# Optimization experiments

Measured on AMD Instinct MI355X. Metric: run time of the kernel, lower is better.

## Reference

```python
import jax, jax.numpy as jnp
import numpy as np

N = 50000   # nodes
E = 800000  # edges (before self-loops)
B = 256     # graphs in batch
F = 128     # input feature dim
H = 4       # heads per layer
C = 64      # out_channels per head
NEG_SLOPE = 0.2


def setup_inputs() -> dict:
    key = jax.random.key(0)
    ks = jax.random.split(key, 16)
    s = 0.05
    inp = {
        "x": jax.random.normal(ks[0], (N, F), dtype=jnp.float32),
        "edge_index": jax.random.randint(ks[1], (2, E), 0, N, dtype=jnp.int32),
        "batch": jnp.sort(jax.random.randint(ks[2], (N,), 0, B, dtype=jnp.int32)),
        # layer 1: F -> H*C
        "W1": jax.random.normal(ks[3], (F, H * C), dtype=jnp.float32) * s,
        "as1": jax.random.normal(ks[4], (H, C), dtype=jnp.float32) * s,
        "ad1": jax.random.normal(ks[5], (H, C), dtype=jnp.float32) * s,
        "b1": jnp.zeros((H * C,), dtype=jnp.float32),
        # layer 2: H*C -> H*C
        "W2": jax.random.normal(ks[6], (H * C, H * C), dtype=jnp.float32) * s,
        "as2": jax.random.normal(ks[7], (H, C), dtype=jnp.float32) * s,
        "ad2": jax.random.normal(ks[8], (H, C), dtype=jnp.float32) * s,
        "b2": jnp.zeros((H * C,), dtype=jnp.float32),
        # layer 3: H*C -> H*C
        "W3": jax.random.normal(ks[9], (H * C, H * C), dtype=jnp.float32) * s,
        "as3": jax.random.normal(ks[10], (H, C), dtype=jnp.float32) * s,
        "ad3": jax.random.normal(ks[11], (H, C), dtype=jnp.float32) * s,
        "b3": jnp.zeros((H * C,), dtype=jnp.float32),
    }
    return inp


def _gat_layer(x, src, dst, W, a_src, a_dst, bias):
    """PyG GATConv (concat=True, self-loops already included in src/dst)."""
    n = x.shape[0]
    xh = (x @ W).reshape(n, H, C)                      # [N,H,C]
    alpha_s = jnp.sum(xh * a_src, axis=-1)             # [N,H]
    alpha_d = jnp.sum(xh * a_dst, axis=-1)             # [N,H]
    logits = alpha_s[src] + alpha_d[dst]               # [E',H]
    logits = jnp.where(logits > 0, logits, NEG_SLOPE * logits)  # LeakyReLU
    # segment-wise softmax over destination neighborhoods
    m = jax.lax.stop_gradient(jax.ops.segment_max(logits, dst, num_segments=n))
    e = jnp.exp(logits - m[dst])
    z = jax.ops.segment_sum(e, dst, num_segments=n)
    alpha = e / (z[dst] + 1e-16)                       # [E',H]
    msg = xh[src] * alpha[:, :, None]                  # [E',H,C]
    out = jax.ops.segment_sum(msg, dst, num_segments=n)  # [N,H,C]
    return out.reshape(n, H * C) + bias


def reference(x, edge_index, batch, W1, as1, ad1, b1, W2, as2, ad2, b2, W3, as3, ad3, b3):
    n = x.shape[0]
    loops = jnp.arange(n, dtype=edge_index.dtype)
    src = jnp.concatenate([edge_index[0], loops])
    dst = jnp.concatenate([edge_index[1], loops])
    # dropout is identity at inference; activation = ReLU between layers
    h = jax.nn.relu(_gat_layer(x, src, dst, W1, as1, ad1, b1))
    h = jax.nn.relu(_gat_layer(h, src, dst, W2, as2, ad2, b2))
    h = _gat_layer(h, src, dst, W3, as3, ad3, b3)
    pooled = jax.ops.segment_max(h, batch, num_segments=B)  # global max pool -> [B, H*C]
    return jnp.squeeze(pooled)
```

## Files before the change

### kernel.cpp

```cpp
#include <hip/hip_runtime.h>
#include <hip/hip_fp16.h>
#include <math.h>

#define NN 50000
#define NE 800000
#define NT 850000
#define NB 256
#define FIN 128
#define HC 256
#define NH 4
#define CD 64
#define NEG 0.2f
#define SCAN_B 196

typedef _Float16 half8 __attribute__((ext_vector_type(8)));
typedef _Float16 half4v __attribute__((ext_vector_type(4)));
typedef float f32x4 __attribute__((ext_vector_type(4)));

__device__ __forceinline__ void gld16(const void* g, void* l) {
    __builtin_amdgcn_global_load_lds(
        (const __attribute__((address_space(1))) void*)g,
        (__attribute__((address_space(3))) void*)l, 16, 0, 0);
}


__global__ void zero_int_kernel(int* __restrict__ p, int n) {
    int i = blockIdx.x * blockDim.x + threadIdx.x;
    if (i < n) p[i] = 0;
}

__global__ void hist_kernel(const int* __restrict__ ei, int* __restrict__ cnt) {
    int e = blockIdx.x * blockDim.x + threadIdx.x;
    if (e < NE) {
        atomicAdd(&cnt[ei[NE + e]], 1);
    } else if (e < NT) {
        atomicAdd(&cnt[e - NE], 1);
    }
}

__global__ __launch_bounds__(256) void part_kernel(const int* __restrict__ cnt,
                                                   int* __restrict__ part) {
    __shared__ int red[4];
    int i = blockIdx.x * 256 + threadIdx.x;
    int v = (i < NN) ? cnt[i] : 0;
#pragma unroll
    for (int off = 32; off > 0; off >>= 1) v += __shfl_down(v, off);
    if ((threadIdx.x & 63) == 0) red[threadIdx.x >> 6] = v;
    __syncthreads();
    if (threadIdx.x == 0) part[blockIdx.x] = red[0] + red[1] + red[2] + red[3];
}

__global__ __launch_bounds__(256) void offs_kernel(const int* __restrict__ part,
                                                   int* __restrict__ boff) {
    __shared__ int sh[256];
    int t = threadIdx.x;
    sh[t] = (t < SCAN_B) ? part[t] : 0;
    __syncthreads();
    for (int off = 1; off < 256; off <<= 1) {
        int add = (t >= off) ? sh[t - off] : 0;
        __syncthreads();
        sh[t] += add;
        __syncthreads();
    }
    boff[t] = (t == 0) ? 0 : sh[t - 1];
}

__global__ __launch_bounds__(256) void write_scan_kernel(const int* __restrict__ cnt,
        const int* __restrict__ boff, int* __restrict__ rowptr, int* __restrict__ cursor) {
    __shared__ int sh[256];
    int t = threadIdx.x;
    int i = blockIdx.x * 256 + t;
    int v = (i < NN) ? cnt[i] : 0;
    sh[t] = v;
    __syncthreads();
    for (int off = 1; off < 256; off <<= 1) {
        int add = (t >= off) ? sh[t - off] : 0;
        __syncthreads();
        sh[t] += add;
        __syncthreads();
    }
    int run = boff[blockIdx.x] + sh[t] - v;
    if (i < NN) { rowptr[i] = run; cursor[i] = run; }
    if (i == NN - 1) rowptr[NN] = run + v;
}

__global__ void scatter_kernel(const int* __restrict__ ei, int* __restrict__ cursor,
                               int* __restrict__ colsrc, int* __restrict__ coldst) {
    int e = blockIdx.x * blockDim.x + threadIdx.x;
    int s, d;
    if (e < NE)      { s = ei[e]; d = ei[NE + e]; }
    else if (e < NT) { s = e - NE; d = s; }
    else return;
    int pos = atomicAdd(&cursor[d], 1);
    colsrc[pos] = s;
    coldst[pos] = d;
}

__global__ void batch_bounds_kernel(const int* __restrict__ batch, int* __restrict__ bstart) {
    int i = blockIdx.x * blockDim.x + threadIdx.x;
    if (i >= NN) return;
    int b = batch[i];
    if (i == 0) {
        for (int bb = 0; bb <= b; ++bb) bstart[bb] = 0;
    } else {
        int pb = batch[i - 1];
        if (pb != b) for (int bb = pb + 1; bb <= b; ++bb) bstart[bb] = i;
    }
    if (i == NN - 1) {
        for (int bb = b + 1; bb <= NB; ++bb) bstart[bb] = NN;
    }
}


__global__ __launch_bounds__(256) void split_x_kernel(const float* __restrict__ X,
        _Float16* __restrict__ Xh, _Float16* __restrict__ Xl) {
    int i = blockIdx.x * 256 + threadIdx.x;
    if (i >= NN * FIN / 4) return;
    float4 v = reinterpret_cast<const float4*>(X)[i];
    half4v h, l;
    h[0] = (_Float16)v.x; h[1] = (_Float16)v.y; h[2] = (_Float16)v.z; h[3] = (_Float16)v.w;
    l[0] = (_Float16)(v.x - (float)h[0]);
    l[1] = (_Float16)(v.y - (float)h[1]);
    l[2] = (_Float16)(v.z - (float)h[2]);
    l[3] = (_Float16)(v.w - (float)h[3]);
    reinterpret_cast<half4v*>(Xh)[i] = h;
    reinterpret_cast<half4v*>(Xl)[i] = l;
}


template<int K>
__global__ __launch_bounds__(256) void wprep_kernel(const float* __restrict__ W,
                                                    _Float16* __restrict__ WtS) {
    __shared__ float sm[8][257];
    const int t = threadIdx.x;
    const int b = blockIdx.x;
    const int kb = b * 8;
    const bool lo3 = (kb >= 2 * K);
    const int kphys = lo3 ? kb - 2 * K : (kb >= K ? kb - K : kb);
#pragma unroll
    for (int i = 0; i < 8; ++i) {
        int idx = i * 256 + t;
        sm[idx >> 8][idx & 255] = W[(size_t)(kphys + (idx >> 8)) * HC + (idx & 255)];
    }
    __syncthreads();
    half8 o;
#pragma unroll
    for (int r = 0; r < 8; ++r) {
        float w = sm[r][t];
        _Float16 h = (_Float16)w;
        o[r] = lo3 ? (_Float16)(w - (float)h) : h;
    }
    *reinterpret_cast<half8*>(&WtS[((size_t)b * 256 + t) * 8]) = o;
}


template<int K>
__global__ __launch_bounds__(256) void mfma_gemm_kernel(
        const _Float16* __restrict__ Xh, const _Float16* __restrict__ Xl,
        const _Float16* __restrict__ WtS, __half* __restrict__ XHo) {
    constexpr int C3 = 3 * K;
    constexpr int NSTEP = C3 / 64;
    __shared__ __align__(16) _Float16 As[2][64 * 64];
    __shared__ __align__(16) _Float16 Bs[2][64 * 256];
    const int t = threadIdx.x;
    const int lane = t & 63;
    const int wid = t >> 6;
    const int wm = wid & 1, wn = wid >> 1;
    const int r0 = blockIdx.x * 64;
    const int l15 = lane & 15;
    const int kcl = lane >> 4;
    const int srowA = t >> 3;
    const int skcA  = t & 7;

    f32x4 acc[2][8];
#pragma unroll
    for (int i = 0; i < 2; ++i)
#pragma unroll
        for (int j = 0; j < 8; ++j) acc[i][j] = (f32x4)0.f;

    auto loadA = [&](int s, float4& a0, float4& a1) {
        const int ks = s * 64;
        const _Float16* src = (ks < K) ? Xh : (ks < 2 * K) ? Xl : Xh;
        const int cbase = (ks < K) ? ks : (ks < 2 * K) ? ks - K : ks - 2 * K;
        a0 = *reinterpret_cast<const float4*>(src + (size_t)(r0 + srowA) * K + cbase + skcA * 8);
        a1 = *reinterpret_cast<const float4*>(src + (size_t)(r0 + 32 + srowA) * K + cbase + skcA * 8);
    };
    auto issueB = [&](int s, int buf) {
        const _Float16* bsrc = WtS + (size_t)s * (64 * 256);
#pragma unroll
        for (int r = 0; r < 8; ++r)
            gld16(bsrc + (r * 256 + t) * 8, &Bs[buf][(r * 256 + t) * 8]);
    };

    float4 va0, va1, vb0, vb1;
    loadA(0, va0, va1);
    issueB(0, 0);
    *reinterpret_cast<float4*>(&As[0][(skcA * 64 + ((srowA)      ^ skcA)) * 8]) = va0;
    *reinterpret_cast<float4*>(&As[0][(skcA * 64 + ((srowA + 32) ^ skcA)) * 8]) = va1;
    __syncthreads();

    for (int s = 0; s < NSTEP; ++s) {
        const int cur = s & 1, nxt = cur ^ 1;
        const bool more = (s + 1) < NSTEP;
        if (more) {
            loadA(s + 1, vb0, vb1);
            issueB(s + 1, nxt);
        }
#pragma unroll
        for (int kk = 0; kk < 2; ++kk) {
            const int kc = kk * 4 + kcl;
            half8 a0 = *reinterpret_cast<const half8*>(
                &As[cur][(kc * 64 + ((wm * 32      + l15) ^ kc)) * 8]);
            half8 a1 = *reinterpret_cast<const half8*>(
                &As[cur][(kc * 64 + ((wm * 32 + 16 + l15) ^ kc)) * 8]);
            const _Float16* bp = &Bs[cur][(kc * 256 + wn * 128 + l15) * 8];
#pragma unroll
            for (int nf = 0; nf < 8; ++nf) {
                half8 b = *reinterpret_cast<const half8*>(bp + nf * 16 * 8);
                acc[0][nf] = __builtin_amdgcn_mfma_f32_16x16x32_f16(a0, b, acc[0][nf], 0, 0, 0);
                acc[1][nf] = __builtin_amdgcn_mfma_f32_16x16x32_f16(a1, b, acc[1][nf], 0, 0, 0);
            }
        }
        if (more) {
            *reinterpret_cast<float4*>(&As[nxt][(skcA * 64 + ((srowA)      ^ skcA)) * 8]) = vb0;
            *reinterpret_cast<float4*>(&As[nxt][(skcA * 64 + ((srowA + 32) ^ skcA)) * 8]) = vb1;
        }
        asm volatile("s_waitcnt vmcnt(0) lgkmcnt(0)" ::: "memory");
        __builtin_amdgcn_s_barrier();
        __builtin_amdgcn_sched_barrier(0);
    }
    const int rb = r0 + wm * 32 + (lane >> 4) * 4;
    const int cb = wn * 128 + l15;
#pragma unroll
    for (int mf = 0; mf < 2; ++mf)
#pragma unroll
        for (int nf = 0; nf < 8; ++nf)
#pragma unroll
            for (int r = 0; r < 4; ++r) {
                int row = rb + mf * 16 + r;
                if (row < NN)
                    XHo[(size_t)row * HC + cb + nf * 16] = __float2half(acc[mf][nf][r]);
            }
}


__global__ __launch_bounds__(256) void alpha_kernel(const __half* __restrict__ XH,
        const float* __restrict__ as, const float* __restrict__ ad,
        float* __restrict__ aS, float* __restrict__ aD) {
    int r = blockIdx.x * 8 + (threadIdx.x >> 5);
    int g = threadIdx.x & 31;
    int h = g >> 3, sub = g & 7;
    half8 xv = *reinterpret_cast<const half8*>(XH + (size_t)r * HC + h * CD + sub * 8);
    const float* ap = as + h * CD + sub * 8;
    const float* dp = ad + h * CD + sub * 8;
    float s = 0.f, d = 0.f;
#pragma unroll
    for (int e = 0; e < 8; ++e) {
        float v = (float)xv[e];
        s += v * ap[e];
        d += v * dp[e];
    }
#pragma unroll
    for (int off = 1; off < 8; off <<= 1) {
        s += __shfl_xor(s, off);
        d += __shfl_xor(d, off);
    }
    if (sub == 0) { aS[r * NH + h] = s; aD[r * NH + h] = d; }
}


#define LEAKY(v) ((v) > 0.f ? (v) : NEG * (v))

__global__ __launch_bounds__(256) void ew_kernel(const int* __restrict__ colsrc,
        const int* __restrict__ coldst,
        const float* __restrict__ aS, const float* __restrict__ aD,
        float4* __restrict__ wE) {
    int p = blockIdx.x * blockDim.x + threadIdx.x;
    if (p >= NT) return;
    int s = colsrc[p], d = coldst[p];
    float4 sv = *reinterpret_cast<const float4*>(aS + s * 4);
    float4 dv = *reinterpret_cast<const float4*>(aD + d * 4);
    float4 w;
    w.x = __expf(LEAKY(sv.x + dv.x));
    w.y = __expf(LEAKY(sv.y + dv.y));
    w.z = __expf(LEAKY(sv.z + dv.z));
    w.w = __expf(LEAKY(sv.w + dv.w));
    wE[p] = w;
}


template<int RELU, int SPLIT>
__global__ __launch_bounds__(256) void aggregate_kernel(
        const int* __restrict__ rowptr, const int* __restrict__ colsrc,
        const float4* __restrict__ wE, const __half* __restrict__ XH,
        const float* __restrict__ bias, float* __restrict__ OUT,
        __half* __restrict__ OUTh, __half* __restrict__ OUTl) {
    int n = blockIdx.x * 4 + (threadIdx.x >> 6);
    int lane = threadIdx.x & 63;
    bool lo = lane < 32;
    const __half2* xbase = reinterpret_cast<const __half2*>(XH);
    float zl = 0.f, zh = 0.f;
    float al0 = 0.f, al1 = 0.f, ah0 = 0.f, ah1 = 0.f;
    int jb = rowptr[n], je = rowptr[n + 1];
    int j = jb;
    for (; j + 8 <= je; j += 8) {
        int sidx[8];
#pragma unroll
        for (int u = 0; u < 8; ++u) sidx[u] = colsrc[j + u];
        float4 w[8];
#pragma unroll
        for (int u = 0; u < 8; ++u) w[u] = wE[j + u];
        __half2 p[8], q[8];
#pragma unroll
        for (int u = 0; u < 8; ++u) {
            const __half2* xp = xbase + (size_t)sidx[u] * (HC / 2) + lane;
            p[u] = xp[0];
            q[u] = xp[64];
        }
#pragma unroll
        for (int u = 0; u < 8; ++u) {
            float wl = lo ? w[u].x : w[u].y, wh = lo ? w[u].z : w[u].w;
            float2 f = __half22float2(p[u]);
            al0 += wl * f.x; al1 += wl * f.y;
            f = __half22float2(q[u]);
            ah0 += wh * f.x; ah1 += wh * f.y;
            zl += wl; zh += wh;
        }
    }
    for (; j + 4 <= je; j += 4) {
        int sidx[4];
#pragma unroll
        for (int u = 0; u < 4; ++u) sidx[u] = colsrc[j + u];
        float4 w[4];
#pragma unroll
        for (int u = 0; u < 4; ++u) w[u] = wE[j + u];
        __half2 p[4], q[4];
#pragma unroll
        for (int u = 0; u < 4; ++u) {
            const __half2* xp = xbase + (size_t)sidx[u] * (HC / 2) + lane;
            p[u] = xp[0];
            q[u] = xp[64];
        }
#pragma unroll
        for (int u = 0; u < 4; ++u) {
            float wl = lo ? w[u].x : w[u].y, wh = lo ? w[u].z : w[u].w;
            float2 f = __half22float2(p[u]);
            al0 += wl * f.x; al1 += wl * f.y;
            f = __half22float2(q[u]);
            ah0 += wh * f.x; ah1 += wh * f.y;
            zl += wl; zh += wh;
        }
    }
    for (; j < je; ++j) {
        int s0 = colsrc[j];
        float4 w0 = wE[j];
        const __half2* xp = xbase + (size_t)s0 * (HC / 2) + lane;
        __half2 p0 = xp[0], q0 = xp[64];
        float w0l = lo ? w0.x : w0.y, w0h = lo ? w0.z : w0.w;
        float2 f = __half22float2(p0);
        al0 += w0l * f.x; al1 += w0l * f.y;
        f = __half22float2(q0);
        ah0 += w0h * f.x; ah1 += w0h * f.y;
        zl += w0l; zh += w0h;
    }
    float izl = 1.f / (zl + 1e-16f), izh = 1.f / (zh + 1e-16f);
    float2 bl = reinterpret_cast<const float2*>(bias)[lane];
    float2 bh = reinterpret_cast<const float2*>(bias + 128)[lane];
    float o0 = al0 * izl + bl.x;
    float o1 = al1 * izl + bl.y;
    float o2 = ah0 * izh + bh.x;
    float o3 = ah1 * izh + bh.y;
    if (RELU) {
        o0 = fmaxf(o0, 0.f); o1 = fmaxf(o1, 0.f);
        o2 = fmaxf(o2, 0.f); o3 = fmaxf(o3, 0.f);
    }
    if (SPLIT) {
        __half h0 = __float2half(o0), h1 = __float2half(o1);
        __half h2 = __float2half(o2), h3 = __float2half(o3);
        __half2* ph = reinterpret_cast<__half2*>(OUTh + (size_t)n * HC) + lane;
        ph[0]  = __half2(h0, h1);
        ph[64] = __half2(h2, h3);
        __half2* pl = reinterpret_cast<__half2*>(OUTl + (size_t)n * HC) + lane;
        pl[0]  = __half2(__float2half(o0 - __half2float(h0)), __float2half(o1 - __half2float(h1)));
        pl[64] = __half2(__float2half(o2 - __half2float(h2)), __float2half(o3 - __half2float(h3)));
    } else {
        float2* op = reinterpret_cast<float2*>(OUT + (size_t)n * HC) + lane;
        op[0]  = make_float2(o0, o1);
        op[64] = make_float2(o2, o3);
    }
}


__global__ __launch_bounds__(256) void pool_kernel(const float* __restrict__ Hf,
        const int* __restrict__ bstart, float* __restrict__ out) {
    int b = blockIdx.x;
    int c = threadIdx.x;
    int i0 = bstart[b], i1 = bstart[b + 1];
    float m = -INFINITY;
    for (int i = i0; i < i1; ++i) m = fmaxf(m, Hf[(size_t)i * HC + c]);
    out[b * HC + c] = m;
}


extern "C" void kernel_launch(void* const* d_in, const int* in_sizes, int n_in,
                              void* d_out, int out_size, void* d_ws, size_t ws_size,
                              hipStream_t stream) {
    const float* x     = (const float*)d_in[0];
    const int*   ei    = (const int*)d_in[1];
    const int*   batch = (const int*)d_in[2];
    const float* W1  = (const float*)d_in[3];
    const float* as1 = (const float*)d_in[4];
    const float* ad1 = (const float*)d_in[5];
    const float* b1  = (const float*)d_in[6];
    const float* W2  = (const float*)d_in[7];
    const float* as2 = (const float*)d_in[8];
    const float* ad2 = (const float*)d_in[9];
    const float* b2  = (const float*)d_in[10];
    const float* W3  = (const float*)d_in[11];
    const float* as3 = (const float*)d_in[12];
    const float* ad3 = (const float*)d_in[13];
    const float* b3  = (const float*)d_in[14];
    float* out = (float*)d_out;

    __half* Hh  = (__half*)d_ws;
    __half* Hl  = Hh + (size_t)NN * HC;
    __half* XHh = Hl + (size_t)NN * HC;
    _Float16* Xh1 = (_Float16*)Hh;
    _Float16* Xl1 = Xh1 + (size_t)NN * FIN;
    float* bufB = (float*)Hh;
    _Float16* WtS = (_Float16*)(XHh + (size_t)NN * HC);
    float4* wE  = (float4*)(WtS + 768 * 256);
    float*  aS  = (float*)(wE + NT);
    float*  aD  = aS + NN * NH;
    int* cnt    = (int*)(aD + NN * NH);
    int* rowptr = cnt + NN;
    int* cursor = rowptr + (NN + 1);
    int* colsrc = cursor + NN;
    int* coldst = colsrc + NT;
    int* bstart = coldst + NT;
    int* part   = bstart + (NB + 1);
    int* boff   = part + SCAN_B;

    zero_int_kernel<<<(NN + 255) / 256, 256, 0, stream>>>(cnt, NN);
    hist_kernel<<<(NT + 255) / 256, 256, 0, stream>>>(ei, cnt);
    part_kernel<<<SCAN_B, 256, 0, stream>>>(cnt, part);
    offs_kernel<<<1, 256, 0, stream>>>(part, boff);
    write_scan_kernel<<<SCAN_B, 256, 0, stream>>>(cnt, boff, rowptr, cursor);
    scatter_kernel<<<(NT + 255) / 256, 256, 0, stream>>>(ei, cursor, colsrc, coldst);
    batch_bounds_kernel<<<(NN + 255) / 256, 256, 0, stream>>>(batch, bstart);

    const int gemm_grid = (NN + 63) / 64;
    const int node_grid = NN / 4;
    const int edge_grid = (NT + 255) / 256;
    const int alpha_grid = NN / 8;

    split_x_kernel<<<(NN * FIN / 4 + 255) / 256, 256, 0, stream>>>(x, Xh1, Xl1);

    wprep_kernel<FIN><<<3 * FIN / 8, 256, 0, stream>>>(W1, WtS);
    mfma_gemm_kernel<FIN><<<gemm_grid, 256, 0, stream>>>(Xh1, Xl1, WtS, XHh);
    alpha_kernel<<<alpha_grid, 256, 0, stream>>>(XHh, as1, ad1, aS, aD);
    ew_kernel<<<edge_grid, 256, 0, stream>>>(colsrc, coldst, aS, aD, wE);
    aggregate_kernel<1, 1><<<node_grid, 256, 0, stream>>>(rowptr, colsrc, wE, XHh, b1,
                                                          nullptr, Hh, Hl);

    wprep_kernel<HC><<<3 * HC / 8, 256, 0, stream>>>(W2, WtS);
    mfma_gemm_kernel<HC><<<gemm_grid, 256, 0, stream>>>((_Float16*)Hh, (_Float16*)Hl, WtS, XHh);
    alpha_kernel<<<alpha_grid, 256, 0, stream>>>(XHh, as2, ad2, aS, aD);
    ew_kernel<<<edge_grid, 256, 0, stream>>>(colsrc, coldst, aS, aD, wE);
    aggregate_kernel<1, 1><<<node_grid, 256, 0, stream>>>(rowptr, colsrc, wE, XHh, b2,
                                                          nullptr, Hh, Hl);

    wprep_kernel<HC><<<3 * HC / 8, 256, 0, stream>>>(W3, WtS);
    mfma_gemm_kernel<HC><<<gemm_grid, 256, 0, stream>>>((_Float16*)Hh, (_Float16*)Hl, WtS, XHh);
    alpha_kernel<<<alpha_grid, 256, 0, stream>>>(XHh, as3, ad3, aS, aD);
    ew_kernel<<<edge_grid, 256, 0, stream>>>(colsrc, coldst, aS, aD, wE);
    aggregate_kernel<0, 0><<<node_grid, 256, 0, stream>>>(rowptr, colsrc, wE, XHh, b3,
                                                          bufB, nullptr, nullptr);

    pool_kernel<<<NB, 256, 0, stream>>>(bufB, bstart, out);
}
```

Baseline: 487.1 us.

## Fuse attention-logit computation and fp32 input split into larger-tile MFMA GEMM

```diff
diff --git a/kernel.cpp b/kernel.cpp
--- a/kernel.cpp
+++ b/kernel.cpp
@@ -14,7 +14,6 @@
 #define SCAN_B 196
 
 typedef _Float16 half8 __attribute__((ext_vector_type(8)));
-typedef _Float16 half4v __attribute__((ext_vector_type(4)));
 typedef float f32x4 __attribute__((ext_vector_type(4)));
 
 __device__ __forceinline__ void gld16(const void* g, void* l) {
@@ -112,22 +111,6 @@
 }
 
 
-__global__ __launch_bounds__(256) void split_x_kernel(const float* __restrict__ X,
-        _Float16* __restrict__ Xh, _Float16* __restrict__ Xl) {
-    int i = blockIdx.x * 256 + threadIdx.x;
-    if (i >= NN * FIN / 4) return;
-    float4 v = reinterpret_cast<const float4*>(X)[i];
-    half4v h, l;
-    h[0] = (_Float16)v.x; h[1] = (_Float16)v.y; h[2] = (_Float16)v.z; h[3] = (_Float16)v.w;
-    l[0] = (_Float16)(v.x - (float)h[0]);
-    l[1] = (_Float16)(v.y - (float)h[1]);
-    l[2] = (_Float16)(v.z - (float)h[2]);
-    l[3] = (_Float16)(v.w - (float)h[3]);
-    reinterpret_cast<half4v*>(Xh)[i] = h;
-    reinterpret_cast<half4v*>(Xl)[i] = l;
-}
-
-
 template<int K>
 __global__ __launch_bounds__(256) void wprep_kernel(const float* __restrict__ W,
                                                     _Float16* __restrict__ WtS) {
@@ -154,23 +137,27 @@
 }
 
 
-template<int K>
-__global__ __launch_bounds__(256) void mfma_gemm_kernel(
+template<int K, bool F32IN>
+__global__ __launch_bounds__(512) void mfma_gemm_kernel(
         const _Float16* __restrict__ Xh, const _Float16* __restrict__ Xl,
-        const _Float16* __restrict__ WtS, __half* __restrict__ XHo) {
+        const float* __restrict__ Xf,
+        const _Float16* __restrict__ WtS, __half* __restrict__ XHo,
+        const float* __restrict__ as_g, const float* __restrict__ ad_g,
+        float* __restrict__ aS, float* __restrict__ aD) {
     constexpr int C3 = 3 * K;
     constexpr int NSTEP = C3 / 64;
-    __shared__ __align__(16) _Float16 As[2][64 * 64];
+    __shared__ __align__(16) _Float16 As[2][128 * 64];
     __shared__ __align__(16) _Float16 Bs[2][64 * 256];
     const int t = threadIdx.x;
     const int lane = t & 63;
     const int wid = t >> 6;
-    const int wm = wid & 1, wn = wid >> 1;
-    const int r0 = blockIdx.x * 64;
+    const int wm = wid & 3, wn = wid >> 2;
+    const int r0 = blockIdx.x * 128;
     const int l15 = lane & 15;
     const int kcl = lane >> 4;
-    const int srowA = t >> 3;
-    const int skcA  = t & 7;
+    const int srow = t >> 2;
+    const int skc0 = (t & 3) * 2;
+    const int arow = min(r0 + srow, NN - 1);
 
     f32x4 acc[2][8];
 #pragma unroll
@@ -178,41 +165,72 @@
 #pragma unroll
         for (int j = 0; j < 8; ++j) acc[i][j] = (f32x4)0.f;
 
-    auto loadA = [&](int s, float4& a0, float4& a1) {
+    float4 st[4];
+    auto loadA = [&](int s) {
         const int ks = s * 64;
-        const _Float16* src = (ks < K) ? Xh : (ks < 2 * K) ? Xl : Xh;
-        const int cbase = (ks < K) ? ks : (ks < 2 * K) ? ks - K : ks - 2 * K;
-        a0 = *reinterpret_cast<const float4*>(src + (size_t)(r0 + srowA) * K + cbase + skcA * 8);
-        a1 = *reinterpret_cast<const float4*>(src + (size_t)(r0 + 32 + srowA) * K + cbase + skcA * 8);
+        const int sel = (ks < K) ? 0 : (ks < 2 * K) ? 1 : 2;
+        const int cbase = ks - sel * K;
+        if (F32IN) {
+            const float* p = Xf + (size_t)arow * K + cbase + skc0 * 8;
+            st[0] = *reinterpret_cast<const float4*>(p);
+            st[1] = *reinterpret_cast<const float4*>(p + 4);
+            st[2] = *reinterpret_cast<const float4*>(p + 8);
+            st[3] = *reinterpret_cast<const float4*>(p + 12);
+        } else {
+            const _Float16* src = (sel == 1) ? Xl : Xh;
+            const _Float16* p = src + (size_t)arow * K + cbase + skc0 * 8;
+            st[0] = *reinterpret_cast<const float4*>(p);
+            st[1] = *reinterpret_cast<const float4*>(p + 8);
+        }
+    };
+    auto writeA = [&](int buf, int s) {
+        _Float16* d0 = &As[buf][(skc0 * 128 + (srow ^ skc0)) * 8];
+        _Float16* d1 = &As[buf][((skc0 + 1) * 128 + (srow ^ (skc0 + 1))) * 8];
+        if (F32IN) {
+            const int ks = s * 64;
+            const int sel = (ks < K) ? 0 : (ks < 2 * K) ? 1 : 2;
+            const float* f = reinterpret_cast<const float*>(st);
+            half8 h0, h1;
+#pragma unroll
+            for (int e = 0; e < 8; ++e) {
+                float v0 = f[e], v1 = f[8 + e];
+                _Float16 a = (_Float16)v0, b = (_Float16)v1;
+                h0[e] = (sel == 1) ? (_Float16)(v0 - (float)a) : a;
+                h1[e] = (sel == 1) ? (_Float16)(v1 - (float)b) : b;
+            }
+            *reinterpret_cast<half8*>(d0) = h0;
+            *reinterpret_cast<half8*>(d1) = h1;
+        } else {
+            *reinterpret_cast<float4*>(d0) = st[0];
+            *reinterpret_cast<float4*>(d1) = st[1];
+        }
     };
     auto issueB = [&](int s, int buf) {
         const _Float16* bsrc = WtS + (size_t)s * (64 * 256);
 #pragma unroll
-        for (int r = 0; r < 8; ++r)
-            gld16(bsrc + (r * 256 + t) * 8, &Bs[buf][(r * 256 + t) * 8]);
+        for (int r = 0; r < 4; ++r)
+            gld16(bsrc + ((size_t)r * 512 + t) * 8, &Bs[buf][((size_t)r * 512 + t) * 8]);
     };
 
-    float4 va0, va1, vb0, vb1;
-    loadA(0, va0, va1);
+    loadA(0);
     issueB(0, 0);
-    *reinterpret_cast<float4*>(&As[0][(skcA * 64 + ((srowA)      ^ skcA)) * 8]) = va0;
-    *reinterpret_cast<float4*>(&As[0][(skcA * 64 + ((srowA + 32) ^ skcA)) * 8]) = va1;
+    writeA(0, 0);
     __syncthreads();
 
     for (int s = 0; s < NSTEP; ++s) {
         const int cur = s & 1, nxt = cur ^ 1;
         const bool more = (s + 1) < NSTEP;
         if (more) {
-            loadA(s + 1, vb0, vb1);
+            loadA(s + 1);
             issueB(s + 1, nxt);
         }
 #pragma unroll
         for (int kk = 0; kk < 2; ++kk) {
             const int kc = kk * 4 + kcl;
             half8 a0 = *reinterpret_cast<const half8*>(
-                &As[cur][(kc * 64 + ((wm * 32      + l15) ^ kc)) * 8]);
+                &As[cur][(kc * 128 + ((wm * 32      + l15) ^ kc)) * 8]);
             half8 a1 = *reinterpret_cast<const half8*>(
-                &As[cur][(kc * 64 + ((wm * 32 + 16 + l15) ^ kc)) * 8]);
+                &As[cur][(kc * 128 + ((wm * 32 + 16 + l15) ^ kc)) * 8]);
             const _Float16* bp = &Bs[cur][(kc * 256 + wn * 128 + l15) * 8];
 #pragma unroll
             for (int nf = 0; nf < 8; ++nf) {
@@ -222,50 +240,48 @@
             }
         }
         if (more) {
-            *reinterpret_cast<float4*>(&As[nxt][(skcA * 64 + ((srowA)      ^ skcA)) * 8]) = vb0;
-            *reinterpret_cast<float4*>(&As[nxt][(skcA * 64 + ((srowA + 32) ^ skcA)) * 8]) = vb1;
-        }
-        asm volatile("s_waitcnt vmcnt(0) lgkmcnt(0)" ::: "memory");
-        __builtin_amdgcn_s_barrier();
-        __builtin_amdgcn_sched_barrier(0);
-    }
+            writeA(nxt, s + 1);
+            asm volatile("s_waitcnt vmcnt(0) lgkmcnt(0)" ::: "memory");
+            __builtin_amdgcn_s_barrier();
+            __builtin_amdgcn_sched_barrier(0);
+        }
+    }
+
     const int rb = r0 + wm * 32 + (lane >> 4) * 4;
     const int cb = wn * 128 + l15;
+    float asv[8], adv[8];
+#pragma unroll
+    for (int nf = 0; nf < 8; ++nf) {
+        asv[nf] = as_g[cb + nf * 16];
+        adv[nf] = ad_g[cb + nf * 16];
+    }
 #pragma unroll
     for (int mf = 0; mf < 2; ++mf)
 #pragma unroll
-        for (int nf = 0; nf < 8; ++nf)
-#pragma unroll
-            for (int r = 0; r < 4; ++r) {
-                int row = rb + mf * 16 + r;
-                if (row < NN)
+        for (int r = 0; r < 4; ++r) {
+            int row = rb + mf * 16 + r;
+            float s0 = 0.f, s1 = 0.f, d0 = 0.f, d1 = 0.f;
+#pragma unroll
+            for (int nf = 0; nf < 4; ++nf) {
+                float a = acc[mf][nf][r], b = acc[mf][nf + 4][r];
+                s0 += a * asv[nf];     d0 += a * adv[nf];
+                s1 += b * asv[nf + 4]; d1 += b * adv[nf + 4];
+            }
+#pragma unroll
+            for (int off = 1; off < 16; off <<= 1) {
+                s0 += __shfl_xor(s0, off); s1 += __shfl_xor(s1, off);
+                d0 += __shfl_xor(d0, off); d1 += __shfl_xor(d1, off);
+            }
+            if (row < NN) {
+                if (l15 == 0) {
+                    aS[row * 4 + 2 * wn] = s0; aS[row * 4 + 2 * wn + 1] = s1;
+                    aD[row * 4 + 2 * wn] = d0; aD[row * 4 + 2 * wn + 1] = d1;
+                }
+#pragma unroll
+                for (int nf = 0; nf < 8; ++nf)
                     XHo[(size_t)row * HC + cb + nf * 16] = __float2half(acc[mf][nf][r]);
             }
-}
-
-
-__global__ __launch_bounds__(256) void alpha_kernel(const __half* __restrict__ XH,
-        const float* __restrict__ as, const float* __restrict__ ad,
-        float* __restrict__ aS, float* __restrict__ aD) {
-    int r = blockIdx.x * 8 + (threadIdx.x >> 5);
-    int g = threadIdx.x & 31;
-    int h = g >> 3, sub = g & 7;
-    half8 xv = *reinterpret_cast<const half8*>(XH + (size_t)r * HC + h * CD + sub * 8);
-    const float* ap = as + h * CD + sub * 8;
-    const float* dp = ad + h * CD + sub * 8;
-    float s = 0.f, d = 0.f;
-#pragma unroll
-    for (int e = 0; e < 8; ++e) {
-        float v = (float)xv[e];
-        s += v * ap[e];
-        d += v * dp[e];
-    }
-#pragma unroll
-    for (int off = 1; off < 8; off <<= 1) {
-        s += __shfl_xor(s, off);
-        d += __shfl_xor(d, off);
-    }
-    if (sub == 0) { aS[r * NH + h] = s; aD[r * NH + h] = d; }
+        }
 }
 
 
@@ -425,8 +441,6 @@
     __half* Hh  = (__half*)d_ws;
     __half* Hl  = Hh + (size_t)NN * HC;
     __half* XHh = Hl + (size_t)NN * HC;
-    _Float16* Xh1 = (_Float16*)Hh;
-    _Float16* Xl1 = Xh1 + (size_t)NN * FIN;
     float* bufB = (float*)Hh;
     _Float16* WtS = (_Float16*)(XHh + (size_t)NN * HC);
     float4* wE  = (float4*)(WtS + 768 * 256);
@@ -449,30 +463,27 @@
     scatter_kernel<<<(NT + 255) / 256, 256, 0, stream>>>(ei, cursor, colsrc, coldst);
     batch_bounds_kernel<<<(NN + 255) / 256, 256, 0, stream>>>(batch, bstart);
 
-    const int gemm_grid = (NN + 63) / 64;
+    const int gemm_grid = (NN + 127) / 128;
     const int node_grid = NN / 4;
     const int edge_grid = (NT + 255) / 256;
-    const int alpha_grid = NN / 8;
-
-    split_x_kernel<<<(NN * FIN / 4 + 255) / 256, 256, 0, stream>>>(x, Xh1, Xl1);
 
     wprep_kernel<FIN><<<3 * FIN / 8, 256, 0, stream>>>(W1, WtS);
-    mfma_gemm_kernel<FIN><<<gemm_grid, 256, 0, stream>>>(Xh1, Xl1, WtS, XHh);
-    alpha_kernel<<<alpha_grid, 256, 0, stream>>>(XHh, as1, ad1, aS, aD);
+    mfma_gemm_kernel<FIN, true><<<gemm_grid, 512, 0, stream>>>(
+        nullptr, nullptr, x, WtS, XHh, as1, ad1, aS, aD);
     ew_kernel<<<edge_grid, 256, 0, stream>>>(colsrc, coldst, aS, aD, wE);
     aggregate_kernel<1, 1><<<node_grid, 256, 0, stream>>>(rowptr, colsrc, wE, XHh, b1,
                                                           nullptr, Hh, Hl);
 
     wprep_kernel<HC><<<3 * HC / 8, 256, 0, stream>>>(W2, WtS);
-    mfma_gemm_kernel<HC><<<gemm_grid, 256, 0, stream>>>((_Float16*)Hh, (_Float16*)Hl, WtS, XHh);
-    alpha_kernel<<<alpha_grid, 256, 0, stream>>>(XHh, as2, ad2, aS, aD);
+    mfma_gemm_kernel<HC, false><<<gemm_grid, 512, 0, stream>>>(
+        (_Float16*)Hh, (_Float16*)Hl, nullptr, WtS, XHh, as2, ad2, aS, aD);
     ew_kernel<<<edge_grid, 256, 0, stream>>>(colsrc, coldst, aS, aD, wE);
     aggregate_kernel<1, 1><<<node_grid, 256, 0, stream>>>(rowptr, colsrc, wE, XHh, b2,
                                                           nullptr, Hh, Hl);
 
     wprep_kernel<HC><<<3 * HC / 8, 256, 0, stream>>>(W3, WtS);
-    mfma_gemm_kernel<HC><<<gemm_grid, 256, 0, stream>>>((_Float16*)Hh, (_Float16*)Hl, WtS, XHh);
-    alpha_kernel<<<alpha_grid, 256, 0, stream>>>(XHh, as3, ad3, aS, aD);
+    mfma_gemm_kernel<HC, false><<<gemm_grid, 512, 0, stream>>>(
+        (_Float16*)Hh, (_Float16*)Hl, nullptr, WtS, XHh, as3, ad3, aS, aD);
     ew_kernel<<<edge_grid, 256, 0, stream>>>(colsrc, coldst, aS, aD, wE);
     aggregate_kernel<0, 0><<<node_grid, 256, 0, stream>>>(rowptr, colsrc, wE, XHh, b3,
                                                           bufB, nullptr, nullptr);
```

New measurement: 499.0 us. 1.02x slower.
